# Kernel optimization log

Hardware: AMD Instinct MI355X
Metric: run time of the kernel (lower is better)

The kernel has to match this reference:

```python
import jax, jax.numpy as jnp
import numpy as np

N, E = 50000, 400000
NODE_IN, EDGE_IN, HID = 16, 8, 16


def setup_inputs() -> dict:
    key = jax.random.key(0)
    ks = jax.random.split(key, 20)
    s = 0.05
    inp = {
        "x": jax.random.normal(ks[0], (N, NODE_IN), jnp.float32),
        "edge_attr": jax.random.normal(ks[1], (E, EDGE_IN), jnp.float32),
        # edge_nn1: Linear(edge_in, hid) -> ReLU -> Linear(hid, node_in*hid)
        "e1_w1": jax.random.normal(ks[2], (EDGE_IN, HID), jnp.float32) * s,
        "e1_b1": jnp.zeros((HID,), jnp.float32),
        "e1_w2": jax.random.normal(ks[3], (HID, NODE_IN * HID), jnp.float32) * s,
        "e1_b2": jnp.zeros((NODE_IN * HID,), jnp.float32),
        # NNConv1 root weight + bias
        "root1": jax.random.normal(ks[4], (NODE_IN, HID), jnp.float32) * s,
        "bias1": jnp.zeros((HID,), jnp.float32),
        # edge_nn2: Linear(edge_in, hid) -> ReLU -> Linear(hid, hid*hid)
        "e2_w1": jax.random.normal(ks[5], (EDGE_IN, HID), jnp.float32) * s,
        "e2_b1": jnp.zeros((HID,), jnp.float32),
        "e2_w2": jax.random.normal(ks[6], (HID, HID * HID), jnp.float32) * s,
        "e2_b2": jnp.zeros((HID * HID,), jnp.float32),
        # NNConv2 root weight + bias
        "root2": jax.random.normal(ks[7], (HID, HID), jnp.float32) * s,
        "bias2": jnp.zeros((HID,), jnp.float32),
        # q_head
        "q_w": jax.random.normal(ks[8], (HID, 1), jnp.float32) * s,
        "q_b": jnp.zeros((1,), jnp.float32),
        "edge_index": jax.random.randint(ks[9], (2, E), 0, N, jnp.int64),
    }
    return inp


def _nnconv(x, src, dst, edge_attr, w1, b1, w2, b2, root, bias, in_ch, out_ch, n_nodes):
    # edge MLP -> per-edge weight matrix [E, in_ch, out_ch]
    h = jax.nn.relu(edge_attr @ w1 + b1)
    W = (h @ w2 + b2).reshape(-1, in_ch, out_ch)
    # gather source features, per-edge matmul (bmm)
    msg = jnp.einsum('ei,eio->eo', x[src], W)  # [E, out_ch]
    # scatter-mean into target nodes
    summed = jax.ops.segment_sum(msg, dst, num_segments=n_nodes)
    cnt = jax.ops.segment_sum(jnp.ones((dst.shape[0], 1), x.dtype), dst, num_segments=n_nodes)
    agg = summed / jnp.maximum(cnt, 1.0)
    # root transform + bias (NNConv update)
    return agg + x @ root + bias


def reference(x, edge_attr, e1_w1, e1_b1, e1_w2, e1_b2, root1, bias1,
              e2_w1, e2_b1, e2_w2, e2_b2, root2, bias2, q_w, q_b, edge_index):
    src, dst = edge_index[0], edge_index[1]
    h = jax.nn.relu(_nnconv(x, src, dst, edge_attr, e1_w1, e1_b1, e1_w2, e1_b2,
                            root1, bias1, NODE_IN, HID, N))
    h = jax.nn.relu(_nnconv(h, src, dst, edge_attr, e2_w1, e2_b1, e2_w2, e2_b2,
                            root2, bias2, HID, HID, N))
    return (h @ q_w + q_b).squeeze(-1)  # [N]
```

## Files before the change

### kernel.cpp

```cpp
#include <hip/hip_runtime.h>

#define NN 50000
#define NE 400000
#define SCAN_N (2 * NN)
#define SA_BLOCKS ((SCAN_N + 255) / 256)
#define YSTRIDE 276


__global__ __launch_bounds__(256) void hist2_kernel(
    const int* __restrict__ eidx, int* __restrict__ cnt)
{
    int e = blockIdx.x * 256 + threadIdx.x;
    if (e < NE) {
        atomicAdd(&cnt[eidx[e]], 1);
        atomicAdd(&cnt[NN + eidx[NE + e]], 1);
    }
}

template <int NT>
__device__ __forceinline__ int block_excl_scan(int v, int tid)
{
    __shared__ int wsum[NT / 64];
    int lane = tid & 63, w = tid >> 6;
    int incl = v;
#pragma unroll
    for (int d = 1; d < 64; d <<= 1) {
        int t = __shfl_up(incl, d, 64);
        if (lane >= d) incl += t;
    }
    if (lane == 63) wsum[w] = incl;
    __syncthreads();
    if (tid == 0) {
        int s = 0;
#pragma unroll
        for (int k = 0; k < NT / 64; ++k) { int t = wsum[k]; wsum[k] = s; s += t; }
    }
    __syncthreads();
    return incl - v + wsum[w];
}

__global__ __launch_bounds__(256) void scan_a_kernel(
    const int* __restrict__ cnt, int* __restrict__ bsum)
{
    __shared__ int wsum[4];
    int tid = threadIdx.x;
    int i = blockIdx.x * 256 + tid;
    int v = (i < SCAN_N) ? cnt[i] : 0;
#pragma unroll
    for (int d = 32; d >= 1; d >>= 1) v += __shfl_down(v, d, 64);
    if ((tid & 63) == 0) wsum[tid >> 6] = v;
    __syncthreads();
    if (tid == 0) bsum[blockIdx.x] = wsum[0] + wsum[1] + wsum[2] + wsum[3];
}

__global__ __launch_bounds__(512) void scan_b_kernel(
    int* __restrict__ bsum, int* __restrict__ offs_all)
{
    int tid = threadIdx.x;
    int v = (tid < SA_BLOCKS) ? bsum[tid] : 0;
    int excl = block_excl_scan<512>(v, tid);
    if (tid < SA_BLOCKS) bsum[tid] = excl;
    if (tid == SA_BLOCKS - 1) offs_all[SCAN_N] = excl + v;
}

__global__ __launch_bounds__(256) void scan_c_kernel(
    int* __restrict__ cnt ,
    const int* __restrict__ bsum, int* __restrict__ offs_all)
{
    int tid = threadIdx.x;
    int i = blockIdx.x * 256 + tid;
    int v = (i < SCAN_N) ? cnt[i] : 0;
    int excl = block_excl_scan<256>(v, tid) + bsum[blockIdx.x];
    if (i < SCAN_N) { offs_all[i] = excl; cnt[i] = excl; }
}

__global__ __launch_bounds__(256) void fill2_kernel(
    const int* __restrict__ eidx, int* __restrict__ cursor,
    int2* __restrict__ ordsrc)
{
    int e = blockIdx.x * 256 + threadIdx.x;
    if (e < NE) {
        int s = eidx[e], d = eidx[NE + e];
        int ps = atomicAdd(&cursor[s], 1);
        int pd = atomicAdd(&cursor[NN + d], 1) - NE;
        ordsrc[ps] = make_int2(e, pd);
    }
}

__global__ __launch_bounds__(256) void edge_fused_kernel(
    const float* __restrict__ xin,
    const float* __restrict__ ea,
    const int2*  __restrict__ ordsrc,
    const int*   __restrict__ offs_src,
    const float* __restrict__ w1,
    const float* __restrict__ b1,
    const float* __restrict__ w2,
    const float* __restrict__ b2,
    float* __restrict__ msg)
{
    __shared__ float xl[16 * 16];
    __shared__ float Yl[16 * YSTRIDE];
    __shared__ int so[17];

    int tid = threadIdx.x;
    int n0 = blockIdx.x * 16;

    {
        int node = tid >> 4, i = tid & 15;
        xl[tid] = xin[(size_t)(n0 + node) * 16 + i];
    }
    if (tid < 17) so[tid] = offs_src[n0 + tid];
    __syncthreads();

    int o = tid & 15;
    {
        int k = tid >> 4;
        float w[16];
#pragma unroll
        for (int i = 0; i < 16; ++i) w[i] = w2[k * 256 + i * 16 + o];
#pragma unroll 4
        for (int node = 0; node < 16; ++node) {
            const float4* xr = (const float4*)&xl[node * 16];
            float4 x0 = xr[0], x1 = xr[1], x2 = xr[2], x3 = xr[3];
            float acc = x0.x * w[0] + x0.y * w[1] + x0.z * w[2] + x0.w * w[3]
                      + x1.x * w[4] + x1.y * w[5] + x1.z * w[6] + x1.w * w[7]
                      + x2.x * w[8] + x2.y * w[9] + x2.z * w[10] + x2.w * w[11]
                      + x3.x * w[12] + x3.y * w[13] + x3.z * w[14] + x3.w * w[15];
            Yl[node * YSTRIDE + k * 16 + o] = acc;
        }
    }
    {
        int node = tid >> 4;
        float w[16];
#pragma unroll
        for (int i = 0; i < 16; ++i) w[i] = b2[i * 16 + o];
        const float4* xr = (const float4*)&xl[node * 16];
        float4 x0 = xr[0], x1 = xr[1], x2 = xr[2], x3 = xr[3];
        float acc = x0.x * w[0] + x0.y * w[1] + x0.z * w[2] + x0.w * w[3]
                  + x1.x * w[4] + x1.y * w[5] + x1.z * w[6] + x1.w * w[7]
                  + x2.x * w[8] + x2.y * w[9] + x2.z * w[10] + x2.w * w[11]
                  + x3.x * w[12] + x3.y * w[13] + x3.z * w[14] + x3.w * w[15];
        Yl[node * YSTRIDE + 256 + o] = acc;
    }
    __syncthreads();

    int j0 = so[0], j1 = so[16];
    for (int j = j0 + tid; j < j1; j += 256) {
        int node = 0;
#pragma unroll
        for (int t = 1; t < 16; ++t) node += (j >= so[t]) ? 1 : 0;

        int2 od = ordsrc[j];
        int e = od.x, pd = od.y;

        const float4* av = (const float4*)(ea + (size_t)e * 8);
        float4 a0 = av[0], a1 = av[1];
        float a[8] = {a0.x, a0.y, a0.z, a0.w, a1.x, a1.y, a1.z, a1.w};

        float hid[16];
#pragma unroll
        for (int jj = 0; jj < 16; ++jj) hid[jj] = b1[jj];
#pragma unroll
        for (int c = 0; c < 8; ++c)
#pragma unroll
            for (int jj = 0; jj < 16; ++jj) hid[jj] += a[c] * w1[c * 16 + jj];
#pragma unroll
        for (int jj = 0; jj < 16; ++jj) hid[jj] = fmaxf(hid[jj], 0.0f);

        const float4* Yr = (const float4*)&Yl[node * YSTRIDE];
        float4 m0 = Yr[64], m1 = Yr[65], m2 = Yr[66], m3 = Yr[67];
#pragma unroll
        for (int k = 0; k < 16; ++k) {
            float hk = hid[k];
            float4 y0 = Yr[k * 4 + 0], y1 = Yr[k * 4 + 1];
            float4 y2 = Yr[k * 4 + 2], y3 = Yr[k * 4 + 3];
            m0.x = fmaf(hk, y0.x, m0.x); m0.y = fmaf(hk, y0.y, m0.y);
            m0.z = fmaf(hk, y0.z, m0.z); m0.w = fmaf(hk, y0.w, m0.w);
            m1.x = fmaf(hk, y1.x, m1.x); m1.y = fmaf(hk, y1.y, m1.y);
            m1.z = fmaf(hk, y1.z, m1.z); m1.w = fmaf(hk, y1.w, m1.w);
            m2.x = fmaf(hk, y2.x, m2.x); m2.y = fmaf(hk, y2.y, m2.y);
            m2.z = fmaf(hk, y2.z, m2.z); m2.w = fmaf(hk, y2.w, m2.w);
            m3.x = fmaf(hk, y3.x, m3.x); m3.y = fmaf(hk, y3.y, m3.y);
            m3.z = fmaf(hk, y3.z, m3.z); m3.w = fmaf(hk, y3.w, m3.w);
        }
        float4* mp = (float4*)(msg + (size_t)pd * 16);
        mp[0] = m0; mp[1] = m1; mp[2] = m2; mp[3] = m3;
    }
}

__global__ __launch_bounds__(256) void node1_gather(
    const float* __restrict__ x, const float* __restrict__ msg,
    const int* __restrict__ offs_dst,
    const float* __restrict__ root, const float* __restrict__ bias,
    float* __restrict__ out)
{
    int t = blockIdx.x * 256 + threadIdx.x;
    int n = t >> 4, o = t & 15;
    if (n >= NN) return;

    int j0 = offs_dst[n] - NE, j1 = offs_dst[n + 1] - NE;
    float sum = 0.0f;
    for (int j = j0; j < j1; ++j) sum += msg[(size_t)j * 16 + o];
    float inv = 1.0f / (float)((j1 - j0) > 0 ? (j1 - j0) : 1);
    float acc = sum * inv + bias[o];

    float xo = x[(size_t)n * 16 + o];
#pragma unroll
    for (int i = 0; i < 16; ++i)
        acc += __shfl(xo, i, 16) * root[i * 16 + o];

    out[(size_t)n * 16 + o] = fmaxf(acc, 0.0f);
}

__global__ __launch_bounds__(256) void node2q_gather(
    const float* __restrict__ h1, const float* __restrict__ msg,
    const int* __restrict__ offs_dst,
    const float* __restrict__ root, const float* __restrict__ bias,
    const float* __restrict__ qw, const float* __restrict__ qb,
    float* __restrict__ out)
{
    int t = blockIdx.x * 256 + threadIdx.x;
    int n = t >> 4, o = t & 15;
    if (n >= NN) return;

    int j0 = offs_dst[n] - NE, j1 = offs_dst[n + 1] - NE;
    float sum = 0.0f;
    for (int j = j0; j < j1; ++j) sum += msg[(size_t)j * 16 + o];
    float inv = 1.0f / (float)((j1 - j0) > 0 ? (j1 - j0) : 1);
    float acc = sum * inv + bias[o];

    float xo = h1[(size_t)n * 16 + o];
#pragma unroll
    for (int i = 0; i < 16; ++i)
        acc += __shfl(xo, i, 16) * root[i * 16 + o];

    float q = fmaxf(acc, 0.0f) * qw[o];
#pragma unroll
    for (int d = 8; d >= 1; d >>= 1) q += __shfl_down(q, d, 16);
    if (o == 0) out[n] = q + qb[0];
}

extern "C" void kernel_launch(void* const* d_in, const int* in_sizes, int n_in,
                              void* d_out, int out_size, void* d_ws, size_t ws_size,
                              hipStream_t stream) {
    const float* x     = (const float*)d_in[0];
    const float* ea    = (const float*)d_in[1];
    const float* e1w1  = (const float*)d_in[2];
    const float* e1b1  = (const float*)d_in[3];
    const float* e1w2  = (const float*)d_in[4];
    const float* e1b2  = (const float*)d_in[5];
    const float* root1 = (const float*)d_in[6];
    const float* bias1 = (const float*)d_in[7];
    const float* e2w1  = (const float*)d_in[8];
    const float* e2b1  = (const float*)d_in[9];
    const float* e2w2  = (const float*)d_in[10];
    const float* e2b2  = (const float*)d_in[11];
    const float* root2 = (const float*)d_in[12];
    const float* bias2 = (const float*)d_in[13];
    const float* qw    = (const float*)d_in[14];
    const float* qb    = (const float*)d_in[15];
    const int*   eidx  = (const int*)d_in[16];

    float* msg      = (float*)d_ws;
    float* h1       = msg + (size_t)16 * NE;
    int*   offs_all = (int*)(h1 + (size_t)16 * NN);
    int*   cursor   = offs_all + SCAN_N + 1;
    int2*  ordsrc   = (int2*)(cursor + SCAN_N);
    int*   bsum     = (int*)(ordsrc + NE);

    int eblocks = (NE + 255) / 256;
    int gblocks = NN / 16;
    int nblocks = (NN * 16 + 255) / 256;

    hipMemsetAsync(cursor, 0, (size_t)SCAN_N * sizeof(int), stream);
    hist2_kernel<<<eblocks, 256, 0, stream>>>(eidx, cursor);
    scan_a_kernel<<<SA_BLOCKS, 256, 0, stream>>>(cursor, bsum);
    scan_b_kernel<<<1, 512, 0, stream>>>(bsum, offs_all);
    scan_c_kernel<<<SA_BLOCKS, 256, 0, stream>>>(cursor, bsum, offs_all);
    fill2_kernel<<<eblocks, 256, 0, stream>>>(eidx, cursor, ordsrc);

    edge_fused_kernel<<<gblocks, 256, 0, stream>>>(x, ea, ordsrc, offs_all,
                                                   e1w1, e1b1, e1w2, e1b2, msg);
    node1_gather<<<nblocks, 256, 0, stream>>>(x, msg, offs_all + NN, root1,
                                              bias1, h1);

    edge_fused_kernel<<<gblocks, 256, 0, stream>>>(h1, ea, ordsrc, offs_all,
                                                   e2w1, e2b1, e2w2, e2b2, msg);
    node2q_gather<<<nblocks, 256, 0, stream>>>(h1, msg, offs_all + NN, root2,
                                               bias2, qw, qb, (float*)d_out);
}
```

Baseline: 254.6 us.

## Fuse layer-1 node gather into layer-2 edge kernel, 32 nodes per block

Removes the separate node1_gather launch by computing h1 for each block's nodes inside the layer-2 edge kernel, writing h1 to shared memory and to global memory. Blocks now cover 32 nodes instead of 16, which amortizes the per-block Y precompute. The per-edge node lookup changes from a 16-way compare loop to a shared-memory slot-to-node table, capped at 1024 slots. A second msg buffer keeps layer-1 messages intact while layer-2 reads them. The risks are more shared memory per block, a serial per-thread fill of the slot table, and possible overflow if a block's source-edge range exceeds 1024.

```diff
diff --git a/kernel.cpp b/kernel.cpp
--- a/kernel.cpp
+++ b/kernel.cpp
@@ -4,7 +4,9 @@
 #define NE 400000
 #define SCAN_N (2 * NN)
 #define SA_BLOCKS ((SCAN_N + 255) / 256)
+#define NPB 32
 #define YSTRIDE 276
+#define MAXSLOT 1024
 
 
 __global__ __launch_bounds__(256) void hist2_kernel(
@@ -64,8 +66,8 @@
 }
 
 __global__ __launch_bounds__(256) void scan_c_kernel(
-    int* __restrict__ cnt ,
-    const int* __restrict__ bsum, int* __restrict__ offs_all)
+    int* __restrict__ cnt, const int* __restrict__ bsum,
+    int* __restrict__ offs_all)
 {
     int tid = threadIdx.x;
     int i = blockIdx.x * 256 + tid;
@@ -87,69 +89,66 @@
     }
 }
 
-__global__ __launch_bounds__(256) void edge_fused_kernel(
-    const float* __restrict__ xin,
+struct FusedSmem {
+    float xl[NPB * 16];
+    float Yl[NPB * YSTRIDE];
+    int so[NPB + 1];
+    unsigned char slotnode[MAXSLOT];
+};
+
+__device__ __forceinline__ void fused_core(
+    FusedSmem& sm, int tid, int nmax,
     const float* __restrict__ ea,
-    const int2*  __restrict__ ordsrc,
-    const int*   __restrict__ offs_src,
-    const float* __restrict__ w1,
-    const float* __restrict__ b1,
-    const float* __restrict__ w2,
-    const float* __restrict__ b2,
-    float* __restrict__ msg)
-{
-    __shared__ float xl[16 * 16];
-    __shared__ float Yl[16 * YSTRIDE];
-    __shared__ int so[17];
-
-    int tid = threadIdx.x;
-    int n0 = blockIdx.x * 16;
-
-    {
-        int node = tid >> 4, i = tid & 15;
-        xl[tid] = xin[(size_t)(n0 + node) * 16 + i];
-    }
-    if (tid < 17) so[tid] = offs_src[n0 + tid];
-    __syncthreads();
-
+    const int2* __restrict__ ordsrc,
+    const float* __restrict__ w1, const float* __restrict__ b1,
+    const float* __restrict__ w2, const float* __restrict__ b2,
+    float* __restrict__ msg_out)
+{
     int o = tid & 15;
+
+    if (tid < nmax) {
+        int a = sm.so[tid] - sm.so[0], b = sm.so[tid + 1] - sm.so[0];
+        for (int j = a; j < b; ++j) sm.slotnode[j] = (unsigned char)tid;
+    }
+
     {
         int k = tid >> 4;
         float w[16];
 #pragma unroll
         for (int i = 0; i < 16; ++i) w[i] = w2[k * 256 + i * 16 + o];
-#pragma unroll 4
-        for (int node = 0; node < 16; ++node) {
-            const float4* xr = (const float4*)&xl[node * 16];
+        for (int node = 0; node < nmax; ++node) {
+            const float4* xr = (const float4*)&sm.xl[node * 16];
             float4 x0 = xr[0], x1 = xr[1], x2 = xr[2], x3 = xr[3];
             float acc = x0.x * w[0] + x0.y * w[1] + x0.z * w[2] + x0.w * w[3]
                       + x1.x * w[4] + x1.y * w[5] + x1.z * w[6] + x1.w * w[7]
                       + x2.x * w[8] + x2.y * w[9] + x2.z * w[10] + x2.w * w[11]
                       + x3.x * w[12] + x3.y * w[13] + x3.z * w[14] + x3.w * w[15];
-            Yl[node * YSTRIDE + k * 16 + o] = acc;
+            sm.Yl[node * YSTRIDE + k * 16 + o] = acc;
         }
     }
     {
-        int node = tid >> 4;
         float w[16];
 #pragma unroll
         for (int i = 0; i < 16; ++i) w[i] = b2[i * 16 + o];
-        const float4* xr = (const float4*)&xl[node * 16];
-        float4 x0 = xr[0], x1 = xr[1], x2 = xr[2], x3 = xr[3];
-        float acc = x0.x * w[0] + x0.y * w[1] + x0.z * w[2] + x0.w * w[3]
-                  + x1.x * w[4] + x1.y * w[5] + x1.z * w[6] + x1.w * w[7]
-                  + x2.x * w[8] + x2.y * w[9] + x2.z * w[10] + x2.w * w[11]
-                  + x3.x * w[12] + x3.y * w[13] + x3.z * w[14] + x3.w * w[15];
-        Yl[node * YSTRIDE + 256 + o] = acc;
-    }
-    __syncthreads();
-
-    int j0 = so[0], j1 = so[16];
+#pragma unroll
+        for (int p = 0; p < 2; ++p) {
+            int node = p * 16 + (tid >> 4);
+            if (node < nmax) {
+                const float4* xr = (const float4*)&sm.xl[node * 16];
+                float4 x0 = xr[0], x1 = xr[1], x2 = xr[2], x3 = xr[3];
+                float acc = x0.x * w[0] + x0.y * w[1] + x0.z * w[2] + x0.w * w[3]
+                          + x1.x * w[4] + x1.y * w[5] + x1.z * w[6] + x1.w * w[7]
+                          + x2.x * w[8] + x2.y * w[9] + x2.z * w[10] + x2.w * w[11]
+                          + x3.x * w[12] + x3.y * w[13] + x3.z * w[14] + x3.w * w[15];
+                sm.Yl[node * YSTRIDE + 256 + o] = acc;
+            }
+        }
+    }
+    __syncthreads();
+
+    int j0 = sm.so[0], j1 = sm.so[nmax];
     for (int j = j0 + tid; j < j1; j += 256) {
-        int node = 0;
-#pragma unroll
-        for (int t = 1; t < 16; ++t) node += (j >= so[t]) ? 1 : 0;
-
+        int node = sm.slotnode[j - j0];
         int2 od = ordsrc[j];
         int e = od.x, pd = od.y;
 
@@ -167,7 +166,7 @@
 #pragma unroll
         for (int jj = 0; jj < 16; ++jj) hid[jj] = fmaxf(hid[jj], 0.0f);
 
-        const float4* Yr = (const float4*)&Yl[node * YSTRIDE];
+        const float4* Yr = (const float4*)&sm.Yl[node * YSTRIDE];
         float4 m0 = Yr[64], m1 = Yr[65], m2 = Yr[66], m3 = Yr[67];
 #pragma unroll
         for (int k = 0; k < 16; ++k) {
@@ -183,33 +182,83 @@
             m3.x = fmaf(hk, y3.x, m3.x); m3.y = fmaf(hk, y3.y, m3.y);
             m3.z = fmaf(hk, y3.z, m3.z); m3.w = fmaf(hk, y3.w, m3.w);
         }
-        float4* mp = (float4*)(msg + (size_t)pd * 16);
+        float4* mp = (float4*)(msg_out + (size_t)pd * 16);
         mp[0] = m0; mp[1] = m1; mp[2] = m2; mp[3] = m3;
     }
 }
 
-__global__ __launch_bounds__(256) void node1_gather(
-    const float* __restrict__ x, const float* __restrict__ msg,
-    const int* __restrict__ offs_dst,
-    const float* __restrict__ root, const float* __restrict__ bias,
-    float* __restrict__ out)
-{
-    int t = blockIdx.x * 256 + threadIdx.x;
-    int n = t >> 4, o = t & 15;
-    if (n >= NN) return;
-
-    int j0 = offs_dst[n] - NE, j1 = offs_dst[n + 1] - NE;
-    float sum = 0.0f;
-    for (int j = j0; j < j1; ++j) sum += msg[(size_t)j * 16 + o];
-    float inv = 1.0f / (float)((j1 - j0) > 0 ? (j1 - j0) : 1);
-    float acc = sum * inv + bias[o];
-
-    float xo = x[(size_t)n * 16 + o];
-#pragma unroll
-    for (int i = 0; i < 16; ++i)
-        acc += __shfl(xo, i, 16) * root[i * 16 + o];
-
-    out[(size_t)n * 16 + o] = fmaxf(acc, 0.0f);
+__global__ __launch_bounds__(256, 4) void edge_fused1(
+    const float* __restrict__ xin, const float* __restrict__ ea,
+    const int2* __restrict__ ordsrc, const int* __restrict__ offs_src,
+    const float* __restrict__ w1, const float* __restrict__ b1,
+    const float* __restrict__ w2, const float* __restrict__ b2,
+    float* __restrict__ msg1)
+{
+    __shared__ FusedSmem sm;
+    int tid = threadIdx.x;
+    int n0 = blockIdx.x * NPB;
+    int nmax = NN - n0; if (nmax > NPB) nmax = NPB;
+
+#pragma unroll
+    for (int p = 0; p < 2; ++p) {
+        int idx = p * 256 + tid;
+        int node = idx >> 4, i = idx & 15;
+        int gn = n0 + node;
+        sm.xl[idx] = (gn < NN) ? xin[(size_t)gn * 16 + i] : 0.0f;
+    }
+    if (tid <= NPB) {
+        int idx = n0 + tid; if (idx > NN) idx = NN;
+        sm.so[tid] = offs_src[idx];
+    }
+    __syncthreads();
+
+    fused_core(sm, tid, nmax, ea, ordsrc, w1, b1, w2, b2, msg1);
+}
+
+__global__ __launch_bounds__(256, 4) void edge_fused2(
+    const float* __restrict__ xin,
+    const float* __restrict__ msg1,
+    const int*  __restrict__ offs_dst,
+    const float* __restrict__ root1, const float* __restrict__ bias1,
+    float* __restrict__ h1g,
+    const float* __restrict__ ea,
+    const int2* __restrict__ ordsrc, const int* __restrict__ offs_src,
+    const float* __restrict__ w1, const float* __restrict__ b1,
+    const float* __restrict__ w2, const float* __restrict__ b2,
+    float* __restrict__ msg2)
+{
+    __shared__ FusedSmem sm;
+    int tid = threadIdx.x;
+    int n0 = blockIdx.x * NPB;
+    int nmax = NN - n0; if (nmax > NPB) nmax = NPB;
+    int o = tid & 15;
+
+#pragma unroll
+    for (int p = 0; p < 2; ++p) {
+        int node = p * 16 + (tid >> 4);
+        int gn = n0 + node;
+        if (gn < NN) {
+            int j0 = offs_dst[gn] - NE, j1 = offs_dst[gn + 1] - NE;
+            float sum = 0.0f;
+            for (int j = j0; j < j1; ++j) sum += msg1[(size_t)j * 16 + o];
+            float inv = 1.0f / (float)((j1 - j0) > 0 ? (j1 - j0) : 1);
+            float acc = sum * inv + bias1[o];
+            float xo = xin[(size_t)gn * 16 + o];
+#pragma unroll
+            for (int i = 0; i < 16; ++i)
+                acc += __shfl(xo, i, 16) * root1[i * 16 + o];
+            float h = fmaxf(acc, 0.0f);
+            sm.xl[node * 16 + o] = h;
+            h1g[(size_t)gn * 16 + o] = h;
+        }
+    }
+    if (tid <= NPB) {
+        int idx = n0 + tid; if (idx > NN) idx = NN;
+        sm.so[tid] = offs_src[idx];
+    }
+    __syncthreads();
+
+    fused_core(sm, tid, nmax, ea, ordsrc, w1, b1, w2, b2, msg2);
 }
 
 __global__ __launch_bounds__(256) void node2q_gather(
@@ -261,15 +310,16 @@
     const float* qb    = (const float*)d_in[15];
     const int*   eidx  = (const int*)d_in[16];
 
-    float* msg      = (float*)d_ws;
-    float* h1       = msg + (size_t)16 * NE;
+    float* msg1     = (float*)d_ws;
+    float* msg2     = msg1 + (size_t)16 * NE;
+    float* h1       = msg2 + (size_t)16 * NE;
     int*   offs_all = (int*)(h1 + (size_t)16 * NN);
     int*   cursor   = offs_all + SCAN_N + 1;
     int2*  ordsrc   = (int2*)(cursor + SCAN_N);
     int*   bsum     = (int*)(ordsrc + NE);
 
     int eblocks = (NE + 255) / 256;
-    int gblocks = NN / 16;
+    int gblocks = (NN + NPB - 1) / NPB;
     int nblocks = (NN * 16 + 255) / 256;
 
     hipMemsetAsync(cursor, 0, (size_t)SCAN_N * sizeof(int), stream);
@@ -279,13 +329,11 @@
     scan_c_kernel<<<SA_BLOCKS, 256, 0, stream>>>(cursor, bsum, offs_all);
     fill2_kernel<<<eblocks, 256, 0, stream>>>(eidx, cursor, ordsrc);
 
-    edge_fused_kernel<<<gblocks, 256, 0, stream>>>(x, ea, ordsrc, offs_all,
-                                                   e1w1, e1b1, e1w2, e1b2, msg);
-    node1_gather<<<nblocks, 256, 0, stream>>>(x, msg, offs_all + NN, root1,
-                                              bias1, h1);
-
-    edge_fused_kernel<<<gblocks, 256, 0, stream>>>(h1, ea, ordsrc, offs_all,
-                                                   e2w1, e2b1, e2w2, e2b2, msg);
-    node2q_gather<<<nblocks, 256, 0, stream>>>(h1, msg, offs_all + NN, root2,
+    edge_fused1<<<gblocks, 256, 0, stream>>>(x, ea, ordsrc, offs_all,
+                                             e1w1, e1b1, e1w2, e1b2, msg1);
+    edge_fused2<<<gblocks, 256, 0, stream>>>(x, msg1, offs_all + NN, root1,
+                                             bias1, h1, ea, ordsrc, offs_all,
+                                             e2w1, e2b1, e2w2, e2b2, msg2);
+    node2q_gather<<<nblocks, 256, 0, stream>>>(h1, msg2, offs_all + NN, root2,
                                                bias2, qw, qb, (float*)d_out);
 }
```

Result: slower. 279.2 us (+9.7%).

## Replace multi-pass scan with atomic-allocated CSR and per-block source buckets

Applied to the files above, without the earlier changes.

Replaces the three-kernel prefix scan with a single alloc kernel in which each block scans locally and claims a global range through an atomicAdd, so destination segments are contiguous but no longer ordered. Source edges are bucketed per 16-node block, and the local node index is packed into the high bits of the edge id, which removes the per-edge search over offsets. Node gathers use base plus degree and two accumulators, and the second layer writes to a separate message buffer. This cuts kernel launches and serial scan work, at the cost of a nondeterministic edge order and an edge id limited to 19 bits.

```diff
diff --git a/kernel.cpp b/kernel.cpp
--- a/kernel.cpp
+++ b/kernel.cpp
@@ -2,18 +2,20 @@
 
 #define NN 50000
 #define NE 400000
-#define SCAN_N (2 * NN)
-#define SA_BLOCKS ((SCAN_N + 255) / 256)
+#define NPB 16
+#define NSB (NN / NPB)
 #define YSTRIDE 276
-
-
-__global__ __launch_bounds__(256) void hist2_kernel(
-    const int* __restrict__ eidx, int* __restrict__ cnt)
+#define DST_BLKS ((NN + 255) / 256)
+
+
+__global__ __launch_bounds__(256) void hist_kernel(
+    const int* __restrict__ eidx, int* __restrict__ dstdeg,
+    int* __restrict__ srcblkcnt)
 {
     int e = blockIdx.x * 256 + threadIdx.x;
     if (e < NE) {
-        atomicAdd(&cnt[eidx[e]], 1);
-        atomicAdd(&cnt[NN + eidx[NE + e]], 1);
+        atomicAdd(&srcblkcnt[eidx[e] >> 4], 1);
+        atomicAdd(&dstdeg[eidx[NE + e]], 1);
     }
 }
 
@@ -39,94 +41,69 @@
     return incl - v + wsum[w];
 }
 
-__global__ __launch_bounds__(256) void scan_a_kernel(
-    const int* __restrict__ cnt, int* __restrict__ bsum)
-{
-    __shared__ int wsum[4];
+__global__ __launch_bounds__(256) void alloc_kernel(
+    const int* __restrict__ dstdeg, const int* __restrict__ srcblkcnt,
+    int* __restrict__ gcur,
+    int* __restrict__ base_dst, int* __restrict__ cur_dst,
+    int* __restrict__ base_src, int* __restrict__ cur_src)
+{
+    __shared__ int base_s;
     int tid = threadIdx.x;
-    int i = blockIdx.x * 256 + tid;
-    int v = (i < SCAN_N) ? cnt[i] : 0;
-#pragma unroll
-    for (int d = 32; d >= 1; d >>= 1) v += __shfl_down(v, d, 64);
-    if ((tid & 63) == 0) wsum[tid >> 6] = v;
-    __syncthreads();
-    if (tid == 0) bsum[blockIdx.x] = wsum[0] + wsum[1] + wsum[2] + wsum[3];
-}
-
-__global__ __launch_bounds__(512) void scan_b_kernel(
-    int* __restrict__ bsum, int* __restrict__ offs_all)
-{
-    int tid = threadIdx.x;
-    int v = (tid < SA_BLOCKS) ? bsum[tid] : 0;
-    int excl = block_excl_scan<512>(v, tid);
-    if (tid < SA_BLOCKS) bsum[tid] = excl;
-    if (tid == SA_BLOCKS - 1) offs_all[SCAN_N] = excl + v;
-}
-
-__global__ __launch_bounds__(256) void scan_c_kernel(
-    int* __restrict__ cnt ,
-    const int* __restrict__ bsum, int* __restrict__ offs_all)
-{
-    int tid = threadIdx.x;
-    int i = blockIdx.x * 256 + tid;
-    int v = (i < SCAN_N) ? cnt[i] : 0;
-    int excl = block_excl_scan<256>(v, tid) + bsum[blockIdx.x];
-    if (i < SCAN_N) { offs_all[i] = excl; cnt[i] = excl; }
-}
-
-__global__ __launch_bounds__(256) void fill2_kernel(
-    const int* __restrict__ eidx, int* __restrict__ cursor,
-    int2* __restrict__ ordsrc)
+    bool isdst = blockIdx.x < DST_BLKS;
+    int i = isdst ? blockIdx.x * 256 + tid : (blockIdx.x - DST_BLKS) * 256 + tid;
+    int v = 0;
+    if (isdst) { if (i < NN) v = dstdeg[i]; }
+    else       { if (i < NSB) v = srcblkcnt[i]; }
+    int excl = block_excl_scan<256>(v, tid);
+    if (tid == 255) base_s = atomicAdd(isdst ? &gcur[0] : &gcur[1], excl + v);
+    __syncthreads();
+    int base = base_s + excl;
+    if (isdst) { if (i < NN)  { base_dst[i] = base; cur_dst[i] = base; } }
+    else       { if (i < NSB) { base_src[i] = base; cur_src[i] = base; } }
+}
+
+__global__ __launch_bounds__(256) void fill_kernel(
+    const int* __restrict__ eidx, int* __restrict__ cur_dst,
+    int* __restrict__ cur_src, int2* __restrict__ ordsrc)
 {
     int e = blockIdx.x * 256 + threadIdx.x;
     if (e < NE) {
         int s = eidx[e], d = eidx[NE + e];
-        int ps = atomicAdd(&cursor[s], 1);
-        int pd = atomicAdd(&cursor[NN + d], 1) - NE;
-        ordsrc[ps] = make_int2(e, pd);
-    }
-}
-
-__global__ __launch_bounds__(256) void edge_fused_kernel(
-    const float* __restrict__ xin,
+        int ps = atomicAdd(&cur_src[s >> 4], 1);
+        int pd = atomicAdd(&cur_dst[d], 1);
+        ordsrc[ps] = make_int2(e | ((s & 15) << 19), pd);
+    }
+}
+
+struct FusedSmem {
+    float xl[NPB * 16];
+    float Yl[NPB * YSTRIDE];
+};
+
+__device__ __forceinline__ void fused_core(
+    FusedSmem& sm, int tid, int j0, int j1,
     const float* __restrict__ ea,
-    const int2*  __restrict__ ordsrc,
-    const int*   __restrict__ offs_src,
-    const float* __restrict__ w1,
-    const float* __restrict__ b1,
-    const float* __restrict__ w2,
-    const float* __restrict__ b2,
-    float* __restrict__ msg)
-{
-    __shared__ float xl[16 * 16];
-    __shared__ float Yl[16 * YSTRIDE];
-    __shared__ int so[17];
-
-    int tid = threadIdx.x;
-    int n0 = blockIdx.x * 16;
-
-    {
-        int node = tid >> 4, i = tid & 15;
-        xl[tid] = xin[(size_t)(n0 + node) * 16 + i];
-    }
-    if (tid < 17) so[tid] = offs_src[n0 + tid];
-    __syncthreads();
-
+    const int2* __restrict__ ordsrc,
+    const float* __restrict__ w1, const float* __restrict__ b1,
+    const float* __restrict__ w2, const float* __restrict__ b2,
+    float* __restrict__ msg_out)
+{
     int o = tid & 15;
+
     {
         int k = tid >> 4;
         float w[16];
 #pragma unroll
         for (int i = 0; i < 16; ++i) w[i] = w2[k * 256 + i * 16 + o];
 #pragma unroll 4
-        for (int node = 0; node < 16; ++node) {
-            const float4* xr = (const float4*)&xl[node * 16];
+        for (int node = 0; node < NPB; ++node) {
+            const float4* xr = (const float4*)&sm.xl[node * 16];
             float4 x0 = xr[0], x1 = xr[1], x2 = xr[2], x3 = xr[3];
             float acc = x0.x * w[0] + x0.y * w[1] + x0.z * w[2] + x0.w * w[3]
                       + x1.x * w[4] + x1.y * w[5] + x1.z * w[6] + x1.w * w[7]
                       + x2.x * w[8] + x2.y * w[9] + x2.z * w[10] + x2.w * w[11]
                       + x3.x * w[12] + x3.y * w[13] + x3.z * w[14] + x3.w * w[15];
-            Yl[node * YSTRIDE + k * 16 + o] = acc;
+            sm.Yl[node * YSTRIDE + k * 16 + o] = acc;
         }
     }
     {
@@ -134,24 +111,21 @@
         float w[16];
 #pragma unroll
         for (int i = 0; i < 16; ++i) w[i] = b2[i * 16 + o];
-        const float4* xr = (const float4*)&xl[node * 16];
+        const float4* xr = (const float4*)&sm.xl[node * 16];
         float4 x0 = xr[0], x1 = xr[1], x2 = xr[2], x3 = xr[3];
         float acc = x0.x * w[0] + x0.y * w[1] + x0.z * w[2] + x0.w * w[3]
                   + x1.x * w[4] + x1.y * w[5] + x1.z * w[6] + x1.w * w[7]
                   + x2.x * w[8] + x2.y * w[9] + x2.z * w[10] + x2.w * w[11]
                   + x3.x * w[12] + x3.y * w[13] + x3.z * w[14] + x3.w * w[15];
-        Yl[node * YSTRIDE + 256 + o] = acc;
-    }
-    __syncthreads();
-
-    int j0 = so[0], j1 = so[16];
+        sm.Yl[node * YSTRIDE + 256 + o] = acc;
+    }
+    __syncthreads();
+
     for (int j = j0 + tid; j < j1; j += 256) {
-        int node = 0;
-#pragma unroll
-        for (int t = 1; t < 16; ++t) node += (j >= so[t]) ? 1 : 0;
-
         int2 od = ordsrc[j];
-        int e = od.x, pd = od.y;
+        int e = od.x & 0x7FFFF;
+        int node = od.x >> 19;
+        int pd = od.y;
 
         const float4* av = (const float4*)(ea + (size_t)e * 8);
         float4 a0 = av[0], a1 = av[1];
@@ -167,7 +141,7 @@
 #pragma unroll
         for (int jj = 0; jj < 16; ++jj) hid[jj] = fmaxf(hid[jj], 0.0f);
 
-        const float4* Yr = (const float4*)&Yl[node * YSTRIDE];
+        const float4* Yr = (const float4*)&sm.Yl[node * YSTRIDE];
         float4 m0 = Yr[64], m1 = Yr[65], m2 = Yr[66], m3 = Yr[67];
 #pragma unroll
         for (int k = 0; k < 16; ++k) {
@@ -183,14 +157,34 @@
             m3.x = fmaf(hk, y3.x, m3.x); m3.y = fmaf(hk, y3.y, m3.y);
             m3.z = fmaf(hk, y3.z, m3.z); m3.w = fmaf(hk, y3.w, m3.w);
         }
-        float4* mp = (float4*)(msg + (size_t)pd * 16);
+        float4* mp = (float4*)(msg_out + (size_t)pd * 16);
         mp[0] = m0; mp[1] = m1; mp[2] = m2; mp[3] = m3;
     }
+}
+
+__global__ __launch_bounds__(256, 4) void edge_fused(
+    const float* __restrict__ xin, const float* __restrict__ ea,
+    const int2* __restrict__ ordsrc,
+    const int* __restrict__ base_src, const int* __restrict__ srcblkcnt,
+    const float* __restrict__ w1, const float* __restrict__ b1,
+    const float* __restrict__ w2, const float* __restrict__ b2,
+    float* __restrict__ msg)
+{
+    __shared__ FusedSmem sm;
+    int tid = threadIdx.x;
+    int n0 = blockIdx.x * NPB;
+
+    sm.xl[tid] = xin[(size_t)n0 * 16 + tid];
+    int j0 = base_src[blockIdx.x];
+    int j1 = j0 + srcblkcnt[blockIdx.x];
+    __syncthreads();
+
+    fused_core(sm, tid, j0, j1, ea, ordsrc, w1, b1, w2, b2, msg);
 }
 
 __global__ __launch_bounds__(256) void node1_gather(
     const float* __restrict__ x, const float* __restrict__ msg,
-    const int* __restrict__ offs_dst,
+    const int* __restrict__ base_dst, const int* __restrict__ dstdeg,
     const float* __restrict__ root, const float* __restrict__ bias,
     float* __restrict__ out)
 {
@@ -198,11 +192,16 @@
     int n = t >> 4, o = t & 15;
     if (n >= NN) return;
 
-    int j0 = offs_dst[n] - NE, j1 = offs_dst[n + 1] - NE;
-    float sum = 0.0f;
-    for (int j = j0; j < j1; ++j) sum += msg[(size_t)j * 16 + o];
-    float inv = 1.0f / (float)((j1 - j0) > 0 ? (j1 - j0) : 1);
-    float acc = sum * inv + bias[o];
+    int j0 = base_dst[n], deg = dstdeg[n], j1 = j0 + deg;
+    float s0 = 0.0f, s1 = 0.0f;
+    int j = j0;
+    for (; j + 1 < j1; j += 2) {
+        s0 += msg[(size_t)j * 16 + o];
+        s1 += msg[(size_t)(j + 1) * 16 + o];
+    }
+    if (j < j1) s0 += msg[(size_t)j * 16 + o];
+    float inv = 1.0f / (float)(deg > 0 ? deg : 1);
+    float acc = (s0 + s1) * inv + bias[o];
 
     float xo = x[(size_t)n * 16 + o];
 #pragma unroll
@@ -214,7 +213,7 @@
 
 __global__ __launch_bounds__(256) void node2q_gather(
     const float* __restrict__ h1, const float* __restrict__ msg,
-    const int* __restrict__ offs_dst,
+    const int* __restrict__ base_dst, const int* __restrict__ dstdeg,
     const float* __restrict__ root, const float* __restrict__ bias,
     const float* __restrict__ qw, const float* __restrict__ qb,
     float* __restrict__ out)
@@ -223,11 +222,16 @@
     int n = t >> 4, o = t & 15;
     if (n >= NN) return;
 
-    int j0 = offs_dst[n] - NE, j1 = offs_dst[n + 1] - NE;
-    float sum = 0.0f;
-    for (int j = j0; j < j1; ++j) sum += msg[(size_t)j * 16 + o];
-    float inv = 1.0f / (float)((j1 - j0) > 0 ? (j1 - j0) : 1);
-    float acc = sum * inv + bias[o];
+    int j0 = base_dst[n], deg = dstdeg[n], j1 = j0 + deg;
+    float s0 = 0.0f, s1 = 0.0f;
+    int j = j0;
+    for (; j + 1 < j1; j += 2) {
+        s0 += msg[(size_t)j * 16 + o];
+        s1 += msg[(size_t)(j + 1) * 16 + o];
+    }
+    if (j < j1) s0 += msg[(size_t)j * 16 + o];
+    float inv = 1.0f / (float)(deg > 0 ? deg : 1);
+    float acc = (s0 + s1) * inv + bias[o];
 
     float xo = h1[(size_t)n * 16 + o];
 #pragma unroll
@@ -261,31 +265,37 @@
     const float* qb    = (const float*)d_in[15];
     const int*   eidx  = (const int*)d_in[16];
 
-    float* msg      = (float*)d_ws;
-    float* h1       = msg + (size_t)16 * NE;
-    int*   offs_all = (int*)(h1 + (size_t)16 * NN);
-    int*   cursor   = offs_all + SCAN_N + 1;
-    int2*  ordsrc   = (int2*)(cursor + SCAN_N);
-    int*   bsum     = (int*)(ordsrc + NE);
+    float* msg1      = (float*)d_ws;
+    float* msg2      = msg1 + (size_t)16 * NE;
+    float* h1        = msg2 + (size_t)16 * NE;
+    int*   dstdeg    = (int*)(h1 + (size_t)16 * NN);
+    int*   srcblkcnt = dstdeg + NN;
+    int*   gcur      = srcblkcnt + NSB;
+    int*   base_dst  = gcur + 2;
+    int*   cur_dst   = base_dst + NN;
+    int*   base_src  = cur_dst + NN;
+    int*   cur_src   = base_src + NSB;
+    int2*  ordsrc    = (int2*)(cur_src + NSB);
 
     int eblocks = (NE + 255) / 256;
-    int gblocks = NN / 16;
+    int ablocks = DST_BLKS + (NSB + 255) / 256;
     int nblocks = (NN * 16 + 255) / 256;
 
-    hipMemsetAsync(cursor, 0, (size_t)SCAN_N * sizeof(int), stream);
-    hist2_kernel<<<eblocks, 256, 0, stream>>>(eidx, cursor);
-    scan_a_kernel<<<SA_BLOCKS, 256, 0, stream>>>(cursor, bsum);
-    scan_b_kernel<<<1, 512, 0, stream>>>(bsum, offs_all);
-    scan_c_kernel<<<SA_BLOCKS, 256, 0, stream>>>(cursor, bsum, offs_all);
-    fill2_kernel<<<eblocks, 256, 0, stream>>>(eidx, cursor, ordsrc);
-
-    edge_fused_kernel<<<gblocks, 256, 0, stream>>>(x, ea, ordsrc, offs_all,
-                                                   e1w1, e1b1, e1w2, e1b2, msg);
-    node1_gather<<<nblocks, 256, 0, stream>>>(x, msg, offs_all + NN, root1,
+    hipMemsetAsync(dstdeg, 0, (size_t)(NN + NSB + 2) * sizeof(int), stream);
+    hist_kernel<<<eblocks, 256, 0, stream>>>(eidx, dstdeg, srcblkcnt);
+    alloc_kernel<<<ablocks, 256, 0, stream>>>(dstdeg, srcblkcnt, gcur,
+                                              base_dst, cur_dst, base_src,
+                                              cur_src);
+    fill_kernel<<<eblocks, 256, 0, stream>>>(eidx, cur_dst, cur_src, ordsrc);
+
+    edge_fused<<<NSB, 256, 0, stream>>>(x, ea, ordsrc, base_src, srcblkcnt,
+                                        e1w1, e1b1, e1w2, e1b2, msg1);
+    node1_gather<<<nblocks, 256, 0, stream>>>(x, msg1, base_dst, dstdeg, root1,
                                               bias1, h1);
 
-    edge_fused_kernel<<<gblocks, 256, 0, stream>>>(h1, ea, ordsrc, offs_all,
-                                                   e2w1, e2b1, e2w2, e2b2, msg);
-    node2q_gather<<<nblocks, 256, 0, stream>>>(h1, msg, offs_all + NN, root2,
-                                               bias2, qw, qb, (float*)d_out);
-}
+    edge_fused<<<NSB, 256, 0, stream>>>(h1, ea, ordsrc, base_src, srcblkcnt,
+                                        e2w1, e2b1, e2w2, e2b2, msg2);
+    node2q_gather<<<nblocks, 256, 0, stream>>>(h1, msg2, base_dst, dstdeg,
+                                               root2, bias2, qw, qb,
+                                               (float*)d_out);
+}
```

New measurement: 306.4 us. 20.4% more time.
